# Optimization experiments

Hardware: AMD Instinct MI355X
Metric: run time of the kernel (lower is better)

The kernel has to match this reference:

```python
import jax, jax.numpy as jnp
import numpy as np

N, M, D = 20000, 16000, 128

def setup_inputs() -> dict:
    key = jax.random.key(0)
    ks = jax.random.split(key, 4)
    return {
        "clear_feature": jax.random.normal(ks[0], (N, D), dtype=jnp.float32),
        "rain_feature": jax.random.normal(ks[1], (M, D), dtype=jnp.float32),
        # torch nn.Linear weight layout: (out_features, in_features)
        "W1": jax.random.normal(ks[2], (D, 2 * D), dtype=jnp.float32) * 0.05,
        "b1": jnp.zeros((D,), dtype=jnp.float32),
        "W2": jax.random.normal(ks[3], (1, D), dtype=jnp.float32) * 0.05,
        "b2": jnp.zeros((1,), dtype=jnp.float32),
    }

def reference(clear_feature, rain_feature, W1, b1, W2, b2):
    # --- KNN alignment (k=1): argmin of squared Euclidean distance == cdist+topk(smallest) ---
    x2 = jnp.sum(clear_feature * clear_feature, axis=-1, keepdims=True)   # [N,1]
    y2 = jnp.sum(rain_feature * rain_feature, axis=-1)                    # [M]
    d2 = x2 + y2 - 2.0 * (clear_feature @ rain_feature.T)                 # [N,M]
    idx = jnp.argmin(d2, axis=-1)                                         # [N]
    aligned = rain_feature[idx]                                           # [N,D] gather
    # --- attention MLP: Linear(2D->D) + ReLU + Linear(D->1) + Sigmoid ---
    comb = jnp.concatenate([clear_feature, aligned], axis=-1)             # [N,2D]
    h = jax.nn.relu(comb @ W1.T + b1)                                     # [N,D]
    w = jax.nn.sigmoid(h @ W2.T + b2)                                     # [N,1]
    # --- gated fusion ---
    return w * clear_feature + (1.0 - w) * aligned
```

## Files before the change

### kernel.cpp

```cpp
#include <hip/hip_runtime.h>
#include <stdint.h>

#define NN 20000
#define MM 16000
#define DD 128
#define CT 500
#define SPLITS 13
#define RB 79

typedef unsigned long long u64;
typedef _Float16 f16x8 __attribute__((ext_vector_type(8)));
typedef float f32x16 __attribute__((ext_vector_type(16)));

__global__ void k_init_keys(u64* keys) {
    int i = blockIdx.x * 256 + threadIdx.x;
    if (i < NN) keys[i] = ~0ull;
}

__global__ void k_y2(const float* __restrict__ rain, float* __restrict__ y2) {
    int row = blockIdx.x * 4 + (threadIdx.x >> 6);
    int lane = threadIdx.x & 63;
    if (row >= MM) return;
    float2 v = ((const float2*)(rain + (size_t)row * DD))[lane];
    float s = v.x * v.x + v.y * v.y;
    #pragma unroll
    for (int off = 32; off > 0; off >>= 1) s += __shfl_down(s, off);
    if (lane == 0) y2[row] = s;
}

__global__ void k_split_A(const float* __restrict__ clear_f,
                          _Float16* __restrict__ Ahi, _Float16* __restrict__ Alo) {
    int id = blockIdx.x * 256 + threadIdx.x;
    if (id >= NN * 16) return;
    int row = id >> 4, kc = id & 15;
    const float4* src = (const float4*)(clear_f + (size_t)row * DD + kc * 8);
    float4 v0 = src[0], v1 = src[1];
    float x[8] = {v0.x, v0.y, v0.z, v0.w, v1.x, v1.y, v1.z, v1.w};
    _Float16 hi[8], lo[8];
    #pragma unroll
    for (int j = 0; j < 8; ++j) {
        float s = -2.f * x[j];
        _Float16 h = (_Float16)s;
        hi[j] = h;
        lo[j] = (_Float16)(s - (float)h);
    }
    *(f16x8*)(Ahi + (size_t)row * DD + (size_t)kc * 8) = *(f16x8*)hi;
    *(f16x8*)(Alo + (size_t)row * DD + (size_t)kc * 8) = *(f16x8*)lo;
}

__global__ void k_split_B(const float* __restrict__ rain, _Float16* __restrict__ Bimg) {
    int id = blockIdx.x * 256 + threadIdx.x;
    if (id >= MM * 16) return;
    int cl = id & 31;
    int kp = (id >> 5) & 15;
    int tc = id >> 9;
    int row = tc * 32 + cl;
    const float4* src = (const float4*)(rain + (size_t)row * DD + kp * 8);
    float4 v0 = src[0], v1 = src[1];
    float x[8] = {v0.x, v0.y, v0.z, v0.w, v1.x, v1.y, v1.z, v1.w};
    _Float16 hi[8], lo[8];
    #pragma unroll
    for (int j = 0; j < 8; ++j) {
        _Float16 h = (_Float16)x[j];
        hi[j] = h;
        lo[j] = (_Float16)(x[j] - (float)h);
    }
    size_t base = (size_t)tc * 8192;
    int chunk = kp * 32 + cl;
    *(f16x8*)(Bimg + base + (size_t)chunk * 8) = *(f16x8*)hi;
    *(f16x8*)(Bimg + base + 4096 + (size_t)chunk * 8) = *(f16x8*)lo;
}

__global__ __launch_bounds__(256, 2) void k_dist(
        const _Float16* __restrict__ Ahi, const _Float16* __restrict__ Alo,
        const _Float16* __restrict__ Bimg, const float* __restrict__ y2,
        u64* __restrict__ keys) {
    __shared__ _Float16 lds[2][8192];

    const int tid = threadIdx.x;
    const int w = tid >> 6, lane = tid & 63;
    const int l5 = lane >> 5, l31 = lane & 31;
    const int split = blockIdx.y;
    const int n0 = blockIdx.x * 256;

    f16x8 afh0[8], afl0[8], afh1[8], afl1[8];
    {
        int r0 = n0 + w * 64 + l31;       if (r0 >= NN) r0 = NN - 1;
        int r1 = n0 + w * 64 + 32 + l31;  if (r1 >= NN) r1 = NN - 1;
        const _Float16* h0 = Ahi + (size_t)r0 * DD + l5 * 8;
        const _Float16* o0 = Alo + (size_t)r0 * DD + l5 * 8;
        const _Float16* h1 = Ahi + (size_t)r1 * DD + l5 * 8;
        const _Float16* o1 = Alo + (size_t)r1 * DD + l5 * 8;
        #pragma unroll
        for (int ks = 0; ks < 8; ++ks) {
            afh0[ks] = *(const f16x8*)(h0 + ks * 16);
            afl0[ks] = *(const f16x8*)(o0 + ks * 16);
            afh1[ks] = *(const f16x8*)(h1 + ks * 16);
            afl1[ks] = *(const f16x8*)(o1 + ks * 16);
        }
    }

    float bestd[32];
    int bestcol[32];
    #pragma unroll
    for (int s = 0; s < 32; ++s) { bestd[s] = 1e30f; bestcol[s] = 0; }

    const int nt = (CT - split + SPLITS - 1) / SPLITS;

    {
        const _Float16* gsrc = Bimg + (size_t)split * 8192;
        #pragma unroll
        for (int n = 0; n < 4; ++n) {
            int seg = w * 4 + n;
            __builtin_amdgcn_global_load_lds(
                (const __attribute__((address_space(1))) unsigned int*)
                    (gsrc + (size_t)seg * 512 + (size_t)lane * 8),
                (__attribute__((address_space(3))) unsigned int*)
                    (&lds[0][0] + (size_t)seg * 512),
                16, 0, 0);
        }
    }
    __syncthreads();

    int p = 0;
    for (int i = 0; i < nt; ++i) {
        const int t = split + i * SPLITS;

        if (i + 1 < nt) {
            const _Float16* gsrc = Bimg + (size_t)(t + SPLITS) * 8192;
            _Float16* lbase = &lds[1 - p][0];
            #pragma unroll
            for (int n = 0; n < 4; ++n) {
                int seg = w * 4 + n;
                __builtin_amdgcn_global_load_lds(
                    (const __attribute__((address_space(1))) unsigned int*)
                        (gsrc + (size_t)seg * 512 + (size_t)lane * 8),
                    (__attribute__((address_space(3))) unsigned int*)
                        (lbase + (size_t)seg * 512),
                    16, 0, 0);
            }
        }

        float y2v = y2[t * 32 + l31];

        f32x16 acc0, acc1;
        #pragma unroll
        for (int e = 0; e < 16; ++e) { acc0[e] = 0.f; acc1[e] = 0.f; }

        const _Float16* lbuf = &lds[p][0];
        #pragma unroll
        for (int ks = 0; ks < 8; ++ks) {
            f16x8 bh = *(const f16x8*)(lbuf + (size_t)ks * 512 + (size_t)lane * 8);
            f16x8 bl = *(const f16x8*)(lbuf + 4096 + (size_t)ks * 512 + (size_t)lane * 8);
            acc0 = __builtin_amdgcn_mfma_f32_32x32x16_f16(afh0[ks], bh, acc0, 0, 0, 0);
            acc1 = __builtin_amdgcn_mfma_f32_32x32x16_f16(afh1[ks], bh, acc1, 0, 0, 0);
            acc0 = __builtin_amdgcn_mfma_f32_32x32x16_f16(afh0[ks], bl, acc0, 0, 0, 0);
            acc1 = __builtin_amdgcn_mfma_f32_32x32x16_f16(afh1[ks], bl, acc1, 0, 0, 0);
            acc0 = __builtin_amdgcn_mfma_f32_32x32x16_f16(afl0[ks], bh, acc0, 0, 0, 0);
            acc1 = __builtin_amdgcn_mfma_f32_32x32x16_f16(afl1[ks], bh, acc1, 0, 0, 0);
        }

        int col = t * 32 + l31;
        #pragma unroll
        for (int e = 0; e < 16; ++e) {
            float d0 = acc0[e] + y2v;
            bool u0 = d0 < bestd[e];
            bestd[e] = u0 ? d0 : bestd[e];
            bestcol[e] = u0 ? col : bestcol[e];
            float d1 = acc1[e] + y2v;
            bool u1 = d1 < bestd[16 + e];
            bestd[16 + e] = u1 ? d1 : bestd[16 + e];
            bestcol[16 + e] = u1 ? col : bestcol[16 + e];
        }

        __syncthreads();
        p ^= 1;
    }

    #pragma unroll
    for (int s = 0; s < 32; ++s) {
        unsigned u = __float_as_uint(bestd[s]);
        u = (u & 0x80000000u) ? ~u : (u | 0x80000000u);
        u64 key = ((u64)u << 32) | (unsigned)bestcol[s];
        #pragma unroll
        for (int off = 1; off < 32; off <<= 1) {
            u64 o = __shfl_xor(key, off);
            if (o < key) key = o;
        }
        if (l31 == 0) {
            int e = s & 15, rb = s >> 4;
            int grow = n0 + w * 64 + rb * 32 + (e & 3) + 8 * (e >> 2) + 4 * l5;
            if (grow < NN) atomicMin(&keys[grow], key);
        }
    }
}

__global__ __launch_bounds__(256) void k_mlp(const float* __restrict__ clear_f,
                                             const float* __restrict__ rain_f,
                                             const float* __restrict__ W1,
                                             const float* __restrict__ b1,
                                             const float* __restrict__ W2,
                                             const float* __restrict__ b2,
                                             const u64* __restrict__ keys,
                                             float* __restrict__ out) {
    __shared__ float comb_s[16][260];
    __shared__ float w1_s[64][133];
    __shared__ float red_s[16][17];
    __shared__ float w_s[16];

    const int tid = threadIdx.x;
    const int n0 = blockIdx.x * 16;

    {
        int r = tid >> 4;
        int t = tid & 15;
        int n = n0 + r;
        unsigned idx = (unsigned)(keys[n] & 0xffffffffu);
        const float4* cp = (const float4*)(clear_f + (size_t)n * DD);
        const float4* rp = (const float4*)(rain_f + (size_t)idx * DD);
        *(float4*)&comb_s[r][4 * t] = cp[t];
        *(float4*)&comb_s[r][4 * (t + 16)] = cp[t + 16];
        *(float4*)&comb_s[r][DD + 4 * t] = rp[t];
        *(float4*)&comb_s[r][DD + 4 * (t + 16)] = rp[t + 16];
    }

    const int r = tid & 15;
    const int g = tid >> 4;
    const int d8 = g * 8;
    float h[8] = {};
    for (int kt = 0; kt < 4; ++kt) {
        __syncthreads();
        #pragma unroll
        for (int i = 0; i < 32; ++i) {
            int lin = i * 256 + tid;
            int kk = lin & 63;
            int d = lin >> 6;
            w1_s[kk][d] = W1[(size_t)d * 256 + kt * 64 + kk];
        }
        __syncthreads();
        #pragma unroll
        for (int kk = 0; kk < 64; ++kk) {
            float c = comb_s[r][kt * 64 + kk];
            float4 wa = *(const float4*)&w1_s[kk][d8];
            float4 wb = *(const float4*)&w1_s[kk][d8 + 4];
            h[0] = fmaf(c, wa.x, h[0]);
            h[1] = fmaf(c, wa.y, h[1]);
            h[2] = fmaf(c, wa.z, h[2]);
            h[3] = fmaf(c, wa.w, h[3]);
            h[4] = fmaf(c, wb.x, h[4]);
            h[5] = fmaf(c, wb.y, h[5]);
            h[6] = fmaf(c, wb.z, h[6]);
            h[7] = fmaf(c, wb.w, h[7]);
        }
    }
    float part = 0.f;
    #pragma unroll
    for (int j = 0; j < 8; ++j) {
        float hv = h[j] + b1[d8 + j];
        hv = hv > 0.f ? hv : 0.f;
        part = fmaf(hv, W2[d8 + j], part);
    }
    red_s[r][g] = part;
    __syncthreads();
    if (tid < 16) {
        float s = 0.f;
        #pragma unroll
        for (int g2 = 0; g2 < 16; ++g2) s += red_s[tid][g2];
        s += b2[0];
        w_s[tid] = 1.f / (1.f + expf(-s));
    }
    __syncthreads();
    {
        int rw = tid >> 4;
        int c8 = (tid & 15) * 8;
        float wv = w_s[rw];
        float ov[8];
        #pragma unroll
        for (int j = 0; j < 8; ++j) {
            float cv = comb_s[rw][c8 + j];
            float av = comb_s[rw][DD + c8 + j];
            ov[j] = wv * cv + (1.f - wv) * av;
        }
        float4* o = (float4*)(out + (size_t)(n0 + rw) * DD + c8);
        o[0] = make_float4(ov[0], ov[1], ov[2], ov[3]);
        o[1] = make_float4(ov[4], ov[5], ov[6], ov[7]);
    }
}

extern "C" void kernel_launch(void* const* d_in, const int* in_sizes, int n_in,
                              void* d_out, int out_size, void* d_ws, size_t ws_size,
                              hipStream_t stream) {
    const float* clear_f = (const float*)d_in[0];
    const float* rain_f = (const float*)d_in[1];
    const float* W1 = (const float*)d_in[2];
    const float* b1 = (const float*)d_in[3];
    const float* W2 = (const float*)d_in[4];
    const float* b2 = (const float*)d_in[5];
    float* out = (float*)d_out;

    char* ws = (char*)d_ws;
    u64* keys = (u64*)ws;
    float* y2 = (float*)(ws + 160000);
    _Float16* Ahi = (_Float16*)(ws + 224000);
    _Float16* Alo = (_Float16*)(ws + 5344000);
    _Float16* Bimg = (_Float16*)(ws + 10464000);

    k_init_keys<<<(NN + 255) / 256, 256, 0, stream>>>(keys);
    k_y2<<<MM / 4, 256, 0, stream>>>(rain_f, y2);
    k_split_A<<<(NN * 16 + 255) / 256, 256, 0, stream>>>(clear_f, Ahi, Alo);
    k_split_B<<<(MM * 16 + 255) / 256, 256, 0, stream>>>(rain_f, Bimg);
    k_dist<<<dim3(RB, SPLITS), 256, 0, stream>>>(Ahi, Alo, Bimg, y2, keys);
    k_mlp<<<NN / 16, 256, 0, stream>>>(clear_f, rain_f, W1, b1, W2, b2, keys, out);
}
```

Before: 393.5 us.

## Triple-buffer B tiles with explicit vmcnt waits, more splits, y2 in LDS

The LDS ring for the distance kernel grows from two to three buffers, prefetching two tiles ahead, and the single __syncthreads becomes explicit s_waitcnt vmcnt plus raw barriers so outstanding loads can stay in flight. The grid goes from 13 to 24 splits and is flattened to 1D with split as the fastest index, so blocks sharing an A row block run next to each other. y2 values are preloaded into LDS and used to seed the accumulators, which removes the per-element add. This adds LDS per block, which may lower occupancy, and the hand-counted vmcnt values must match the number of loads issued.

```diff
diff --git a/kernel.cpp b/kernel.cpp
--- a/kernel.cpp
+++ b/kernel.cpp
@@ -5,7 +5,7 @@
 #define MM 16000
 #define DD 128
 #define CT 500
-#define SPLITS 13
+#define SPLITS 24
 #define RB 79
 
 typedef unsigned long long u64;
@@ -75,13 +75,16 @@
         const _Float16* __restrict__ Ahi, const _Float16* __restrict__ Alo,
         const _Float16* __restrict__ Bimg, const float* __restrict__ y2,
         u64* __restrict__ keys) {
-    __shared__ _Float16 lds[2][8192];
+    __shared__ _Float16 lds[3][8192];
+    __shared__ float y2s[672];
 
     const int tid = threadIdx.x;
     const int w = tid >> 6, lane = tid & 63;
     const int l5 = lane >> 5, l31 = lane & 31;
-    const int split = blockIdx.y;
-    const int n0 = blockIdx.x * 256;
+    const int b = blockIdx.x;
+    const int split = b % SPLITS;
+    const int n0 = (b / SPLITS) * 256;
+    const int nt = (CT - split + SPLITS - 1) / SPLITS;
 
     f16x8 afh0[8], afl0[8], afh1[8], afl1[8];
     {
@@ -100,15 +103,12 @@
         }
     }
 
-    float bestd[32];
-    int bestcol[32];
-    #pragma unroll
-    for (int s = 0; s < 32; ++s) { bestd[s] = 1e30f; bestcol[s] = 0; }
-
-    const int nt = (CT - split + SPLITS - 1) / SPLITS;
-
-    {
-        const _Float16* gsrc = Bimg + (size_t)split * 8192;
+    for (int j = tid; j < nt * 32; j += 256)
+        y2s[j] = y2[(split + (j >> 5) * SPLITS) * 32 + (j & 31)];
+
+    #pragma unroll
+    for (int pi = 0; pi < 2; ++pi) {
+        const _Float16* gsrc = Bimg + (size_t)(split + pi * SPLITS) * 8192;
         #pragma unroll
         for (int n = 0; n < 4; ++n) {
             int seg = w * 4 + n;
@@ -116,19 +116,24 @@
                 (const __attribute__((address_space(1))) unsigned int*)
                     (gsrc + (size_t)seg * 512 + (size_t)lane * 8),
                 (__attribute__((address_space(3))) unsigned int*)
-                    (&lds[0][0] + (size_t)seg * 512),
+                    (&lds[pi][0] + (size_t)seg * 512),
                 16, 0, 0);
         }
     }
     __syncthreads();
+
+    float bestd[32];
+    int bestcol[32];
+    #pragma unroll
+    for (int s = 0; s < 32; ++s) { bestd[s] = 1e30f; bestcol[s] = 0; }
 
     int p = 0;
     for (int i = 0; i < nt; ++i) {
         const int t = split + i * SPLITS;
 
-        if (i + 1 < nt) {
-            const _Float16* gsrc = Bimg + (size_t)(t + SPLITS) * 8192;
-            _Float16* lbase = &lds[1 - p][0];
+        if (i + 2 < nt) {
+            const _Float16* gsrc = Bimg + (size_t)(t + 2 * SPLITS) * 8192;
+            _Float16* dst = &lds[(p + 2) % 3][0];
             #pragma unroll
             for (int n = 0; n < 4; ++n) {
                 int seg = w * 4 + n;
@@ -136,16 +141,22 @@
                     (const __attribute__((address_space(1))) unsigned int*)
                         (gsrc + (size_t)seg * 512 + (size_t)lane * 8),
                     (__attribute__((address_space(3))) unsigned int*)
-                        (lbase + (size_t)seg * 512),
+                        (dst + (size_t)seg * 512),
                     16, 0, 0);
             }
         }
 
-        float y2v = y2[t * 32 + l31];
+        if (i + 2 < nt)      { __asm__ __volatile__("s_waitcnt vmcnt(8)" ::: "memory"); }
+        else if (i + 1 < nt) { __asm__ __volatile__("s_waitcnt vmcnt(4)" ::: "memory"); }
+        else                 { __asm__ __volatile__("s_waitcnt vmcnt(0)" ::: "memory"); }
+        __builtin_amdgcn_s_barrier();
+        __asm__ __volatile__("" ::: "memory");
+
+        float y2v = y2s[i * 32 + l31];
 
         f32x16 acc0, acc1;
         #pragma unroll
-        for (int e = 0; e < 16; ++e) { acc0[e] = 0.f; acc1[e] = 0.f; }
+        for (int e = 0; e < 16; ++e) { acc0[e] = y2v; acc1[e] = y2v; }
 
         const _Float16* lbuf = &lds[p][0];
         #pragma unroll
@@ -163,18 +174,21 @@
         int col = t * 32 + l31;
         #pragma unroll
         for (int e = 0; e < 16; ++e) {
-            float d0 = acc0[e] + y2v;
+            float d0 = acc0[e];
             bool u0 = d0 < bestd[e];
             bestd[e] = u0 ? d0 : bestd[e];
             bestcol[e] = u0 ? col : bestcol[e];
-            float d1 = acc1[e] + y2v;
+            float d1 = acc1[e];
             bool u1 = d1 < bestd[16 + e];
             bestd[16 + e] = u1 ? d1 : bestd[16 + e];
             bestcol[16 + e] = u1 ? col : bestcol[16 + e];
         }
 
-        __syncthreads();
-        p ^= 1;
+        __asm__ __volatile__("" ::: "memory");
+        __builtin_amdgcn_s_barrier();
+        __asm__ __volatile__("" ::: "memory");
+
+        p = (p + 1) % 3;
     }
 
     #pragma unroll
@@ -188,8 +202,8 @@
             if (o < key) key = o;
         }
         if (l31 == 0) {
-            int e = s & 15, rb = s >> 4;
-            int grow = n0 + w * 64 + rb * 32 + (e & 3) + 8 * (e >> 2) + 4 * l5;
+            int e = s & 15, rb2 = s >> 4;
+            int grow = n0 + w * 64 + rb2 * 32 + (e & 3) + 8 * (e >> 2) + 4 * l5;
             if (grow < NN) atomicMin(&keys[grow], key);
         }
     }
@@ -309,6 +323,6 @@
     k_y2<<<MM / 4, 256, 0, stream>>>(rain_f, y2);
     k_split_A<<<(NN * 16 + 255) / 256, 256, 0, stream>>>(clear_f, Ahi, Alo);
     k_split_B<<<(MM * 16 + 255) / 256, 256, 0, stream>>>(rain_f, Bimg);
-    k_dist<<<dim3(RB, SPLITS), 256, 0, stream>>>(Ahi, Alo, Bimg, y2, keys);
+    k_dist<<<RB * SPLITS, 256, 0, stream>>>(Ahi, Alo, Bimg, y2, keys);
     k_mlp<<<NN / 16, 256, 0, stream>>>(clear_f, rain_f, W1, b1, W2, b2, keys, out);
 }
```

After: 381.0 us. -3.2%, faster.
